# Optimization experiments

Measured on AMD Instinct MI355X. Metric: run time of the kernel, lower is better.

## Reference

```python
import math
import jax, jax.numpy as jnp
import numpy as np

HEAD_SIZE = 64
DEPTH = 0

def lambda_init_fn(depth):
    depth = depth + 1
    return 0.8 - 0.6 * math.exp(-0.3 * depth)

def setup_inputs() -> dict:
    key = jax.random.key(0)
    ks = jax.random.split(key, 9)
    B, T, C = 4, 4096, 1024
    H2 = 2 * HEAD_SIZE  # 128
    return {
        "x":  jax.random.normal(ks[0], (B, T, C), dtype=jnp.float32),
        "Wq": jax.random.normal(ks[1], (C, H2), dtype=jnp.float32) * (C ** -0.5),
        "Wk": jax.random.normal(ks[2], (C, H2), dtype=jnp.float32) * (C ** -0.5),
        "Wv": jax.random.normal(ks[3], (C, H2), dtype=jnp.float32) * (C ** -0.5),
        "lambda_q1": jax.random.normal(ks[4], (HEAD_SIZE,), dtype=jnp.float32) * 0.1,
        "lambda_q2": jax.random.normal(ks[5], (HEAD_SIZE,), dtype=jnp.float32) * 0.1,
        "lambda_k1": jax.random.normal(ks[6], (HEAD_SIZE,), dtype=jnp.float32) * 0.1,
        "lambda_k2": jax.random.normal(ks[7], (HEAD_SIZE,), dtype=jnp.float32) * 0.1,
    }

def reference(x, Wq, Wk, Wv, lambda_q1, lambda_q2, lambda_k1, lambda_k2):
    B, T, C = x.shape
    q = x @ Wq  # (B,T,2*hs)
    k = x @ Wk
    v = x @ Wv  # (B,T,2*hs)
    q1, q2 = jnp.split(q, 2, axis=-1)
    k1, k2 = jnp.split(k, 2, axis=-1)
    scale = 1.0 / math.sqrt(HEAD_SIZE)
    w1 = jnp.einsum('btd,bsd->bts', q1, k1) * scale  # (B,T,T)
    w2 = jnp.einsum('btd,bsd->bts', q2, k2) * scale
    causal = jnp.tril(jnp.ones((T, T), dtype=bool))
    neg_inf = jnp.float32(-jnp.inf)
    w1 = jnp.where(causal, w1, neg_inf)
    w2 = jnp.where(causal, w2, neg_inf)
    lam1 = jnp.exp(jnp.sum(lambda_q1 * lambda_k1))
    lam2 = jnp.exp(jnp.sum(lambda_q2 * lambda_k2))
    lam = lam1 - lam2 + lambda_init_fn(DEPTH)
    weights = jax.nn.softmax(w1, axis=-1) - lam * jax.nn.softmax(w2, axis=-1)
    out = jnp.einsum('bts,bsd->btd', weights, v)  # (B,T,2*hs)
    return out
```

## Files before the change

kernel.cpp:

```cpp
#include <hip/hip_runtime.h>
#include <hip/hip_bf16.h>

typedef __bf16 bf16x8 __attribute__((ext_vector_type(8)));
typedef float f32x4 __attribute__((ext_vector_type(4)));

#define LOG2E 1.4426950408889634f
#define LAMBDA_INIT 0.3555090675909693f
#define CEXP 0.18033688011112042f
#define MOFF 11.541560327111708f

#define K_OFF   ((size_t)16384 * 128)
#define VT_OFF  ((size_t)2 * 16384 * 128)
#define PART_OFF_BYTES ((size_t)12582912)
#define WT_OFF_BYTES   ((size_t)46661632)
#define REC_FLOATS 4160

__device__ __forceinline__ unsigned short f2bf(float f) {
    __hip_bfloat16 h = __float2bfloat16(f);
    unsigned short u;
    __builtin_memcpy(&u, &h, 2);
    return u;
}
__device__ __forceinline__ float bf2f(unsigned short u) {
    unsigned int x = ((unsigned int)u) << 16;
    float f;
    __builtin_memcpy(&f, &x, 4);
    return f;
}
__device__ __forceinline__ unsigned int cvt_pk_bf16(float a, float b) {
    unsigned int r;
    asm volatile("v_cvt_pk_bf16_f32 %0, %1, %2" : "=v"(r) : "v"(a), "v"(b));
    return r;
}

__global__ __launch_bounds__(256) void prep_wt(
    const float* __restrict__ Wq, const float* __restrict__ Wk,
    const float* __restrict__ Wv, unsigned short* __restrict__ WT) {
    const int kt = blockIdx.x, nt = blockIdx.y, mat = blockIdx.z;
    const float* W = (mat == 0) ? Wq : (mat == 1) ? Wk : Wv;
    unsigned short* O = WT + (size_t)mat * 128 * 1024;
    __shared__ float tb[64][65];
    const int r = threadIdx.x >> 2, c4 = (threadIdx.x & 3) * 16;
    for (int j = 0; j < 4; ++j) {
        float4 v = *(const float4*)&W[(size_t)(kt * 64 + r) * 128 + nt * 64 + c4 + j * 4];
        tb[r][c4 + j * 4 + 0] = v.x;
        tb[r][c4 + j * 4 + 1] = v.y;
        tb[r][c4 + j * 4 + 2] = v.z;
        tb[r][c4 + j * 4 + 3] = v.w;
    }
    __syncthreads();
    unsigned short tmp[16];
    for (int j = 0; j < 16; ++j) tmp[j] = f2bf(tb[c4 + j][r]);
    *(uint4*)&O[(size_t)(nt * 64 + r) * 1024 + kt * 64 + c4] = *(uint4*)&tmp[0];
    *(uint4*)&O[(size_t)(nt * 64 + r) * 1024 + kt * 64 + c4 + 8] = *(uint4*)&tmp[8];
}

__global__ __launch_bounds__(256) void qkv_gemm(
    const float* __restrict__ x, const unsigned short* __restrict__ WT,
    unsigned short* __restrict__ qkv) {
    const int tid = threadIdx.x;
    const int l = tid & 63, wid = tid >> 6;
    const int g = l >> 4, i16 = l & 15;
    const int row0 = blockIdx.x * 128;
    const int mat = blockIdx.y;
    const unsigned short* Wt = WT + (size_t)mat * 128 * 1024;

    __shared__ unsigned short smem[2][128][72];
    auto xs = smem[0];
    auto wt = smem[1];

    f32x4 acc[2][8];
    const f32x4 z4 = {0.f, 0.f, 0.f, 0.f};
    for (int a = 0; a < 2; ++a)
        for (int b = 0; b < 8; ++b) acc[a][b] = z4;

    for (int k0 = 0; k0 < 1024; k0 += 64) {
        __syncthreads();
        {
            const int c = (tid & 15) * 4;
            const int rbase = tid >> 4;
            #pragma unroll
            for (int it = 0; it < 8; ++it) {
                int r = rbase + it * 16;
                const float4 v = *(const float4*)&x[(size_t)(row0 + r) * 1024 + k0 + c];
                ushort4 pk = make_ushort4(f2bf(v.x), f2bf(v.y), f2bf(v.z), f2bf(v.w));
                *(ushort4*)&xs[r][c] = pk;
            }
        }
        {
            #pragma unroll
            for (int it = 0; it < 4; ++it) {
                int lin = it * 256 + tid;
                int n = lin >> 3, k8 = (lin & 7) * 8;
                *(uint4*)&wt[n][k8] = *(const uint4*)&Wt[(size_t)n * 1024 + k0 + k8];
            }
        }
        __syncthreads();

        bf16x8 af[2][2];
        for (int rb = 0; rb < 2; ++rb)
            for (int c = 0; c < 2; ++c)
                af[rb][c] = *(const bf16x8*)&xs[wid * 32 + rb * 16 + i16][c * 32 + 8 * g];
        for (int nb = 0; nb < 8; ++nb) {
            bf16x8 b0 = *(const bf16x8*)&wt[nb * 16 + i16][8 * g];
            bf16x8 b1 = *(const bf16x8*)&wt[nb * 16 + i16][32 + 8 * g];
            for (int rb = 0; rb < 2; ++rb) {
                acc[rb][nb] = __builtin_amdgcn_mfma_f32_16x16x32_bf16(af[rb][0], b0, acc[rb][nb], 0, 0, 0);
                acc[rb][nb] = __builtin_amdgcn_mfma_f32_16x16x32_bf16(af[rb][1], b1, acc[rb][nb], 0, 0, 0);
            }
        }
    }

    __syncthreads();
    unsigned short(*ts)[136] = (unsigned short(*)[136]) & smem[0][0][0];
    for (int rb = 0; rb < 2; ++rb)
        for (int nb = 0; nb < 8; ++nb)
            for (int r = 0; r < 4; ++r)
                ts[wid * 32 + rb * 16 + g * 4 + r][nb * 16 + i16] = f2bf(acc[rb][nb][r]);
    __syncthreads();
    if (mat < 2) {
        unsigned short* outp = qkv + (size_t)mat * 16384 * 128 + (size_t)row0 * 128;
        #pragma unroll
        for (int it = 0; it < 8; ++it) {
            int tr = it * 16 + (tid >> 4), dv0 = (tid & 15) * 8;
            *(uint4*)&outp[tr * 128 + dv0] = *(const uint4*)&ts[tr][dv0];
        }
    } else {
        unsigned short* vtb = qkv + VT_OFF + (size_t)(row0 >> 12) * 128 * 4096 + (size_t)(row0 & 4095);
        const int dv = tid >> 1, half = tid & 1;
        #pragma unroll
        for (int blk = 0; blk < 8; ++blk) {
            unsigned short tmp[8];
            #pragma unroll
            for (int j = 0; j < 8; ++j) tmp[j] = ts[half * 64 + blk * 8 + j][dv];
            *(uint4*)&vtb[(size_t)dv * 4096 + half * 64 + blk * 8] = *(uint4*)tmp;
        }
    }
}

__global__ __launch_bounds__(256) void diff_attn_pair(
    const unsigned short* __restrict__ q, const unsigned short* __restrict__ kk_,
    const unsigned short* __restrict__ vvt,
    float* __restrict__ part) {
    const int bx = blockIdx.x, b = blockIdx.y;
    const int c = blockIdx.z >> 1, branch = blockIdx.z & 1;

    const int tid = threadIdx.x;
    const int l = tid & 63, w = tid >> 6;
    const int gq = l >> 4, i16 = l & 15;
    const float NEGINF = -__builtin_inff();

    __shared__ unsigned short ks[64][72];
    __shared__ unsigned short vt[128][72];
    __shared__ unsigned short ps[4][16][72];

    const int krow = tid >> 3;
    const int kcol = (tid & 7) * 8;
    const int vrow = tid >> 3;
    const int vcol = (tid & 7) * 8;

    const size_t bbase = (size_t)b * 4096;
    const size_t vbase = (size_t)b * 524288;
    const f32x4 z4 = {0.f, 0.f, 0.f, 0.f};
    uint4 kr0, kr1, vr0, vr1, vr2, vr3;

#define KV_LOAD(s_) do {                                                            \
        const unsigned short* kp = &kk_[(bbase + (size_t)(s_) * 64) * 128 + branch * 64 + kcol]; \
        kr0 = *(const uint4*)&kp[(size_t)(krow +  0) * 128];                        \
        kr1 = *(const uint4*)&kp[(size_t)(krow + 32) * 128];                        \
        const unsigned short* vp = &vvt[vbase + (size_t)(s_) * 64 + vcol];          \
        vr0 = *(const uint4*)&vp[(size_t)(vrow +  0) * 4096];                       \
        vr1 = *(const uint4*)&vp[(size_t)(vrow + 32) * 4096];                       \
        vr2 = *(const uint4*)&vp[(size_t)(vrow + 64) * 4096];                       \
        vr3 = *(const uint4*)&vp[(size_t)(vrow + 96) * 4096];                       \
    } while (0)

#define KV_STORE() do {                                                             \
        *(uint4*)&ks[krow +  0][kcol] = kr0;                                        \
        *(uint4*)&ks[krow + 32][kcol] = kr1;                                        \
        *(uint4*)&vt[vrow +  0][vcol] = vr0;                                        \
        *(uint4*)&vt[vrow + 32][vcol] = vr1;                                        \
        *(uint4*)&vt[vrow + 64][vcol] = vr2;                                        \
        *(uint4*)&vt[vrow + 96][vcol] = vr3;                                        \
    } while (0)

    #pragma unroll 1
    for (int seg = 0; seg < 2; ++seg) {
        const int t = seg ? (63 - bx) : bx;
        const int n = t + 1;
        const int s0 = (c * n) >> 2, smax = ((c + 1) * n) >> 2;

        float* rec = part + ((((size_t)b * 64 + t) * 4 + c) * 2 + branch) * REC_FLOATS;
        if (s0 >= smax) {
            unsigned int* pz = (unsigned int*)rec;
            for (int i = tid; i < REC_FLOATS; i += 256) pz[i] = 0u;
            continue;
        }

        bf16x8 qf[2];
        for (int cc = 0; cc < 2; ++cc)
            qf[cc] = *(const bf16x8*)&q[(bbase + t * 64 + w * 16 + i16) * 128 + branch * 64 + cc * 32 + 8 * gq];

        float lsum = 0.f;
        f32x4 acc_o[8];
        for (int nb = 0; nb < 8; ++nb) acc_o[nb] = z4;

        KV_LOAD(s0);
        #pragma unroll 1
        for (int s = s0; s < smax; ++s) {
            __syncthreads();
            KV_STORE();
            if (s + 1 < smax) KV_LOAD(s + 1);
            __syncthreads();

            f32x4 sc[4];
            for (int cb = 0; cb < 4; ++cb) sc[cb] = z4;
            __builtin_amdgcn_s_setprio(1);
            for (int cb = 0; cb < 4; ++cb)
                for (int cc = 0; cc < 2; ++cc) {
                    bf16x8 kf = *(const bf16x8*)&ks[cb * 16 + i16][cc * 32 + 8 * gq];
                    sc[cb] = __builtin_amdgcn_mfma_f32_16x16x32_bf16(kf, qf[cc], sc[cb], 0, 0, 0);
                }
            __builtin_amdgcn_s_setprio(0);
            if (s == t) {
                int ql = w * 16 + i16;
                for (int cb = 0; cb < 4; ++cb)
                    for (int r = 0; r < 4; ++r)
                        if (cb * 16 + gq * 4 + r > ql) sc[cb][r] = NEGINF;
            }
            #pragma unroll
            for (int cb = 0; cb < 4; ++cb)
                for (int r = 0; r < 4; ++r) {
                    float pv = exp2f(fmaf(sc[cb][r], CEXP, -MOFF));
                    sc[cb][r] = pv;
                    lsum += pv;
                }
            #pragma unroll
            for (int cb = 0; cb < 4; ++cb) {
                uint2 pw;
                pw.x = cvt_pk_bf16(sc[cb][0], sc[cb][1]);
                pw.y = cvt_pk_bf16(sc[cb][2], sc[cb][3]);
                *(uint2*)&ps[w][i16][cb * 16 + gq * 4] = pw;
            }
            asm volatile("s_waitcnt lgkmcnt(0)" ::: "memory");
            bf16x8 pa[2];
            for (int cc = 0; cc < 2; ++cc)
                pa[cc] = *(const bf16x8*)&ps[w][i16][cc * 32 + 8 * gq];
            __builtin_amdgcn_s_setprio(1);
            for (int nb = 0; nb < 8; ++nb)
                for (int cc = 0; cc < 2; ++cc) {
                    bf16x8 vb = *(const bf16x8*)&vt[nb * 16 + i16][cc * 32 + 8 * gq];
                    acc_o[nb] = __builtin_amdgcn_mfma_f32_16x16x32_bf16(pa[cc], vb, acc_o[nb], 0, 0, 0);
                }
            __builtin_amdgcn_s_setprio(0);
        }

        lsum += __shfl_xor(lsum, 16);
        lsum += __shfl_xor(lsum, 32);
        unsigned short* Orec = (unsigned short*)(rec + 64);
        if (gq == 0) rec[w * 16 + i16] = lsum;
        for (int nb = 0; nb < 8; ++nb)
            for (int r = 0; r < 4; ++r) {
                int row = w * 16 + gq * 4 + r;
                Orec[row * 128 + nb * 16 + i16] = f2bf(acc_o[nb][r]);
            }
    }
#undef KV_LOAD
#undef KV_STORE
}

__global__ __launch_bounds__(256) void diff_combine(
    const float* __restrict__ part,
    const float* __restrict__ lq1, const float* __restrict__ lq2,
    const float* __restrict__ lk1, const float* __restrict__ lk2,
    float* __restrict__ out) {
    const int t = blockIdx.x, b = blockIdx.y;
    const int tid = threadIdx.x;
    __shared__ float sl[2][64];
    __shared__ float s_lam;

    const float* recbase = part + (((size_t)b * 64 + t) * 4) * 2 * REC_FLOATS;

    if (tid < 64) {
        float s1 = lq1[tid] * lk1[tid];
        float s2 = lq2[tid] * lk2[tid];
        for (int off = 32; off > 0; off >>= 1) {
            s1 += __shfl_xor(s1, off);
            s2 += __shfl_xor(s2, off);
        }
        if (tid == 0) s_lam = expf(s1) - expf(s2) + LAMBDA_INIT;
    }
    if (tid < 128) {
        int r = tid & 63, br = tid >> 6;
        float acc = 0.f;
        for (int c = 0; c < 4; ++c) acc += recbase[(c * 2 + br) * REC_FLOATS + r];
        sl[br][r] = acc;
    }
    __syncthreads();
    const float lam = s_lam;

    float* op = out + ((size_t)b * 4096 + (size_t)t * 64) * 128;
    for (int grp = 0; grp < 4; ++grp) {
        int gid = grp * 256 + tid;
        int e = gid * 8;
        int row = e >> 7;
        float o1[8] = {0, 0, 0, 0, 0, 0, 0, 0}, o2[8] = {0, 0, 0, 0, 0, 0, 0, 0};
        #pragma unroll
        for (int c = 0; c < 4; ++c) {
            const unsigned short* O0 = (const unsigned short*)(recbase + (c * 2 + 0) * REC_FLOATS + 64);
            const unsigned short* O1 = (const unsigned short*)(recbase + (c * 2 + 1) * REC_FLOATS + 64);
            uint4 u0 = *(const uint4*)&O0[e];
            uint4 u1 = *(const uint4*)&O1[e];
            const unsigned short* e0 = (const unsigned short*)&u0;
            const unsigned short* e1 = (const unsigned short*)&u1;
            #pragma unroll
            for (int j = 0; j < 8; ++j) {
                o1[j] += bf2f(e0[j]);
                o2[j] += bf2f(e1[j]);
            }
        }
        float l1inv = 1.0f / sl[0][row], l2inv = 1.0f / sl[1][row];
        float res[8];
        #pragma unroll
        for (int j = 0; j < 8; ++j) res[j] = o1[j] * l1inv - lam * o2[j] * l2inv;
        *(float4*)&op[e] = *(float4*)&res[0];
        *(float4*)&op[e + 4] = *(float4*)&res[4];
    }
}

extern "C" void kernel_launch(void* const* d_in, const int* in_sizes, int n_in,
                              void* d_out, int out_size, void* d_ws, size_t ws_size,
                              hipStream_t stream) {
    const float* x   = (const float*)d_in[0];
    const float* Wq  = (const float*)d_in[1];
    const float* Wk  = (const float*)d_in[2];
    const float* Wv  = (const float*)d_in[3];
    const float* lq1 = (const float*)d_in[4];
    const float* lq2 = (const float*)d_in[5];
    const float* lk1 = (const float*)d_in[6];
    const float* lk2 = (const float*)d_in[7];
    float* out = (float*)d_out;
    unsigned short* qkv = (unsigned short*)d_ws;
    float* part = (float*)((char*)d_ws + PART_OFF_BYTES);
    unsigned short* WT = (unsigned short*)((char*)d_ws + WT_OFF_BYTES);

    prep_wt<<<dim3(16, 2, 3), 256, 0, stream>>>(Wq, Wk, Wv, WT);
    qkv_gemm<<<dim3(128, 3), 256, 0, stream>>>(x, WT, qkv);

    const unsigned short* qb = qkv;
    const unsigned short* kb = qkv + K_OFF;
    const unsigned short* vtb = qkv + VT_OFF;
    diff_attn_pair<<<dim3(32, 4, 8), 256, 0, stream>>>(qb, kb, vtb, part);
    diff_combine<<<dim3(64, 4), 256, 0, stream>>>(part, lq1, lq2, lk1, lk2, out);
}
```

Baseline: 104.9 us.

## Use fragment-ordered shared-memory layout in attention and reorder QKV GEMM grid

The attention kernel now stores K, V^T and P tiles in shared memory in MFMA-fragment order, so each lane reads its operand with one contiguous 16-byte load at lane*8, with no padded row-major indexing. The goal is fewer bank conflicts and simpler address arithmetic in the inner loop, and the MFMA loops are fully unrolled. The QKV GEMM grid is transposed so the three weight matrices for the same rows run in adjacent blocks, improving L2 reuse of x, and the bf16 packing there uses the packed convert. Global loads for K/V now follow the fragment mapping, which may make global access less coalesced.

New measurement: 147.9 us. +40.9%, slower.

```diff
diff --git a/kernel.cpp b/kernel.cpp
--- a/kernel.cpp
+++ b/kernel.cpp
@@ -61,8 +61,8 @@
     const int tid = threadIdx.x;
     const int l = tid & 63, wid = tid >> 6;
     const int g = l >> 4, i16 = l & 15;
-    const int row0 = blockIdx.x * 128;
-    const int mat = blockIdx.y;
+    const int row0 = blockIdx.y * 128;
+    const int mat = blockIdx.x;
     const unsigned short* Wt = WT + (size_t)mat * 128 * 1024;
 
     __shared__ unsigned short smem[2][128][72];
@@ -83,8 +83,10 @@
             for (int it = 0; it < 8; ++it) {
                 int r = rbase + it * 16;
                 const float4 v = *(const float4*)&x[(size_t)(row0 + r) * 1024 + k0 + c];
-                ushort4 pk = make_ushort4(f2bf(v.x), f2bf(v.y), f2bf(v.z), f2bf(v.w));
-                *(ushort4*)&xs[r][c] = pk;
+                uint2 pk;
+                pk.x = cvt_pk_bf16(v.x, v.y);
+                pk.y = cvt_pk_bf16(v.z, v.w);
+                *(uint2*)&xs[r][c] = pk;
             }
         }
         {
@@ -150,14 +152,25 @@
     const int gq = l >> 4, i16 = l & 15;
     const float NEGINF = -__builtin_inff();
 
-    __shared__ unsigned short ks[64][72];
-    __shared__ unsigned short vt[128][72];
-    __shared__ unsigned short ps[4][16][72];
-
-    const int krow = tid >> 3;
-    const int kcol = (tid & 7) * 8;
-    const int vrow = tid >> 3;
-    const int vcol = (tid & 7) * 8;
+    __shared__ unsigned short ksf[4096];
+    __shared__ unsigned short vtf[8192];
+    __shared__ unsigned short psf[4096];
+
+    const int kgoff = (w * 16 + i16) * 128 + 8 * gq;
+    const int kdst0 = ((w * 2 + 0) * 64 + l) * 8;
+    const int kdst1 = ((w * 2 + 1) * 64 + l) * 8;
+    const int vg0 = (w * 16 + i16) * 4096 + 8 * gq;
+    const int vg2 = ((w + 4) * 16 + i16) * 4096 + 8 * gq;
+    const int vdst0 = ((w * 2 + 0) * 64 + l) * 8;
+    const int vdst1 = ((w * 2 + 1) * 64 + l) * 8;
+    const int vdst2 = (((w + 4) * 2 + 0) * 64 + l) * 8;
+    const int vdst3 = (((w + 4) * 2 + 1) * 64 + l) * 8;
+    int pdst[4];
+    #pragma unroll
+    for (int cb = 0; cb < 4; ++cb)
+        pdst[cb] = ((w * 2 + (cb >> 1)) * 64 + ((cb & 1) * 2 + (gq >> 1)) * 16 + i16) * 8 + (gq & 1) * 4;
+    const int prd0 = ((w * 2 + 0) * 64 + l) * 8;
+    const int prd1 = ((w * 2 + 1) * 64 + l) * 8;
 
     const size_t bbase = (size_t)b * 4096;
     const size_t vbase = (size_t)b * 524288;
@@ -165,23 +178,23 @@
     uint4 kr0, kr1, vr0, vr1, vr2, vr3;
 
 #define KV_LOAD(s_) do {                                                            \
-        const unsigned short* kp = &kk_[(bbase + (size_t)(s_) * 64) * 128 + branch * 64 + kcol]; \
-        kr0 = *(const uint4*)&kp[(size_t)(krow +  0) * 128];                        \
-        kr1 = *(const uint4*)&kp[(size_t)(krow + 32) * 128];                        \
-        const unsigned short* vp = &vvt[vbase + (size_t)(s_) * 64 + vcol];          \
-        vr0 = *(const uint4*)&vp[(size_t)(vrow +  0) * 4096];                       \
-        vr1 = *(const uint4*)&vp[(size_t)(vrow + 32) * 4096];                       \
-        vr2 = *(const uint4*)&vp[(size_t)(vrow + 64) * 4096];                       \
-        vr3 = *(const uint4*)&vp[(size_t)(vrow + 96) * 4096];                       \
+        const unsigned short* kp = &kk_[(bbase + (size_t)(s_) * 64) * 128 + branch * 64]; \
+        kr0 = *(const uint4*)&kp[kgoff];                                            \
+        kr1 = *(const uint4*)&kp[kgoff + 32];                                       \
+        const unsigned short* vp = &vvt[vbase + (size_t)(s_) * 64];                 \
+        vr0 = *(const uint4*)&vp[vg0];                                              \
+        vr1 = *(const uint4*)&vp[vg0 + 32];                                         \
+        vr2 = *(const uint4*)&vp[vg2];                                              \
+        vr3 = *(const uint4*)&vp[vg2 + 32];                                         \
     } while (0)
 
 #define KV_STORE() do {                                                             \
-        *(uint4*)&ks[krow +  0][kcol] = kr0;                                        \
-        *(uint4*)&ks[krow + 32][kcol] = kr1;                                        \
-        *(uint4*)&vt[vrow +  0][vcol] = vr0;                                        \
-        *(uint4*)&vt[vrow + 32][vcol] = vr1;                                        \
-        *(uint4*)&vt[vrow + 64][vcol] = vr2;                                        \
-        *(uint4*)&vt[vrow + 96][vcol] = vr3;                                        \
+        *(uint4*)&ksf[kdst0] = kr0;                                                 \
+        *(uint4*)&ksf[kdst1] = kr1;                                                 \
+        *(uint4*)&vtf[vdst0] = vr0;                                                 \
+        *(uint4*)&vtf[vdst1] = vr1;                                                 \
+        *(uint4*)&vtf[vdst2] = vr2;                                                 \
+        *(uint4*)&vtf[vdst3] = vr3;                                                 \
     } while (0)
 
     #pragma unroll 1
@@ -216,9 +229,10 @@
             f32x4 sc[4];
             for (int cb = 0; cb < 4; ++cb) sc[cb] = z4;
             __builtin_amdgcn_s_setprio(1);
+            #pragma unroll
             for (int cb = 0; cb < 4; ++cb)
                 for (int cc = 0; cc < 2; ++cc) {
-                    bf16x8 kf = *(const bf16x8*)&ks[cb * 16 + i16][cc * 32 + 8 * gq];
+                    bf16x8 kf = *(const bf16x8*)&ksf[((cb * 2 + cc) * 64 + l) * 8];
                     sc[cb] = __builtin_amdgcn_mfma_f32_16x16x32_bf16(kf, qf[cc], sc[cb], 0, 0, 0);
                 }
             __builtin_amdgcn_s_setprio(0);
@@ -240,18 +254,19 @@
                 uint2 pw;
                 pw.x = cvt_pk_bf16(sc[cb][0], sc[cb][1]);
                 pw.y = cvt_pk_bf16(sc[cb][2], sc[cb][3]);
-                *(uint2*)&ps[w][i16][cb * 16 + gq * 4] = pw;
+                *(uint2*)&psf[pdst[cb]] = pw;
             }
             asm volatile("s_waitcnt lgkmcnt(0)" ::: "memory");
-            bf16x8 pa[2];
-            for (int cc = 0; cc < 2; ++cc)
-                pa[cc] = *(const bf16x8*)&ps[w][i16][cc * 32 + 8 * gq];
+            bf16x8 pa0 = *(const bf16x8*)&psf[prd0];
+            bf16x8 pa1 = *(const bf16x8*)&psf[prd1];
             __builtin_amdgcn_s_setprio(1);
-            for (int nb = 0; nb < 8; ++nb)
-                for (int cc = 0; cc < 2; ++cc) {
-                    bf16x8 vb = *(const bf16x8*)&vt[nb * 16 + i16][cc * 32 + 8 * gq];
-                    acc_o[nb] = __builtin_amdgcn_mfma_f32_16x16x32_bf16(pa[cc], vb, acc_o[nb], 0, 0, 0);
-                }
+            #pragma unroll
+            for (int nb = 0; nb < 8; ++nb) {
+                bf16x8 vb0 = *(const bf16x8*)&vtf[((nb * 2 + 0) * 64 + l) * 8];
+                acc_o[nb] = __builtin_amdgcn_mfma_f32_16x16x32_bf16(pa0, vb0, acc_o[nb], 0, 0, 0);
+                bf16x8 vb1 = *(const bf16x8*)&vtf[((nb * 2 + 1) * 64 + l) * 8];
+                acc_o[nb] = __builtin_amdgcn_mfma_f32_16x16x32_bf16(pa1, vb1, acc_o[nb], 0, 0, 0);
+            }
             __builtin_amdgcn_s_setprio(0);
         }
 
@@ -345,7 +360,7 @@
     unsigned short* WT = (unsigned short*)((char*)d_ws + WT_OFF_BYTES);
 
     prep_wt<<<dim3(16, 2, 3), 256, 0, stream>>>(Wq, Wk, Wv, WT);
-    qkv_gemm<<<dim3(128, 3), 256, 0, stream>>>(x, WT, qkv);
+    qkv_gemm<<<dim3(3, 128), 256, 0, stream>>>(x, WT, qkv);
 
     const unsigned short* qb = qkv;
     const unsigned short* kb = qkv + K_OFF;
```
